# Kernel tuning notes

Measured on AMD Instinct MI355X. Metric: run time of the kernel, lower is better.

Reference implementation:

```python
import jax, jax.numpy as jnp
import numpy as np

N_EXPERTS = 6
TOP_K = 2
AUX_COEFF = 0.01
W_SCALE = 0.02  # keep activations in a sane range with random weights


def setup_inputs() -> dict:
    key = jax.random.key(0)
    k1, k2, k3, k4 = jax.random.split(key, 4)
    B, T, D, H = 4, 2048, 1024, 4096
    x = jax.random.normal(k1, (B, T, D), dtype=jnp.float32)
    w_router = jax.random.normal(k2, (D, N_EXPERTS), dtype=jnp.float32) * W_SCALE
    w1 = jax.random.normal(k3, (N_EXPERTS, D, H), dtype=jnp.float32) * W_SCALE
    w2 = jax.random.normal(k4, (N_EXPERTS, H, D), dtype=jnp.float32) * W_SCALE
    return {"x": x, "w_router": w_router, "w1": w1, "w2": w2}


def reference(x, w_router, w1, w2):
    B, T, D = x.shape
    x_flat = x.reshape(-1, D)                              # (N, D)
    router_logits = x_flat @ w_router                      # (N, E)
    router_probs = jax.nn.softmax(router_logits, axis=-1)
    top_probs, top_idx = jax.lax.top_k(router_probs, TOP_K)  # (N, K)
    top_probs = top_probs / jnp.sum(top_probs, axis=-1, keepdims=True)
    # combine weights per (token, expert): sum over k slots hitting expert e
    onehot = jax.nn.one_hot(top_idx, N_EXPERTS, dtype=x.dtype)  # (N, K, E)
    comb = jnp.einsum('nke,nk->ne', onehot, top_probs)          # (N, E)
    out = jnp.zeros_like(x_flat)
    for e in range(N_EXPERTS):
        h = jax.nn.gelu(x_flat @ w1[e], approximate=False)      # (N, H)
        out = out + comb[:, e:e + 1] * (h @ w2[e])              # (N, D)
    tokens_per_expert = jnp.mean(router_probs, axis=0)          # (E,)
    uniform = jnp.full_like(tokens_per_expert, 1.0 / N_EXPERTS)
    aux_loss = AUX_COEFF * jnp.mean((tokens_per_expert - uniform) ** 2)
    return out.reshape(B, T, D), aux_loss
```

## Files before the change

### kernel.cpp

```cpp
#include <hip/hip_runtime.h>

#define N_TOK 8192
#define DDIM  1024
#define HDIM  4096
#define NEXP  6
#define RBLOCKS (N_TOK / 4)
#define SBLOCKS 32

typedef unsigned short ushort_t;
typedef __bf16 bf16_t;
typedef bf16_t bf16x8 __attribute__((ext_vector_type(8)));
typedef float f32x4 __attribute__((ext_vector_type(4)));

typedef const __attribute__((address_space(1))) void* gptr_t;
typedef __attribute__((address_space(3))) void* lptr_t;

__device__ __forceinline__ void g2l16(const void* g, void* l) {
    __builtin_amdgcn_global_load_lds((gptr_t)g, (lptr_t)l, 16, 0, 0);
}

__device__ __forceinline__ ushort_t f2bf(float f) {
    unsigned int u = __float_as_uint(f);
    unsigned int r = (u + 0x7FFFu + ((u >> 16) & 1u)) >> 16;
    return (ushort_t)r;
}

__global__ void transpose_bf16_kernel(const float* __restrict__ src, ushort_t* __restrict__ dst,
                                      int R, int C) {
    __shared__ float tile[32][33];
    size_t msz = (size_t)R * C;
    src += (size_t)blockIdx.z * msz;
    dst += (size_t)blockIdx.z * msz;
    int c0 = blockIdx.x * 32, r0 = blockIdx.y * 32;
    int tx = threadIdx.x & 31, ty = threadIdx.x >> 5;
#pragma unroll
    for (int i = 0; i < 4; ++i)
        tile[ty + 8 * i][tx] = src[(size_t)(r0 + ty + 8 * i) * C + c0 + tx];
    __syncthreads();
#pragma unroll
    for (int i = 0; i < 4; ++i)
        dst[(size_t)(c0 + ty + 8 * i) * R + r0 + tx] = f2bf(tile[tx][ty + 8 * i]);
}

__global__ void router_kernel(const float* __restrict__ x, const float* __restrict__ wr,
                              ushort_t* __restrict__ xb,
                              int* __restrict__ tok_e, float* __restrict__ tok_w,
                              float* __restrict__ part_p, int* __restrict__ part_c) {
    __shared__ float bsum[NEXP];
    __shared__ int bcnt[NEXP];
    int wid = threadIdx.x >> 6, l = threadIdx.x & 63;
    if (threadIdx.x < NEXP) { bsum[threadIdx.x] = 0.f; bcnt[threadIdx.x] = 0; }
    __syncthreads();
    int t = blockIdx.x * 4 + wid;
    const float* xr = x + (size_t)t * DDIM;
    ushort_t* xbr = xb + (size_t)t * DDIM;
    float acc[NEXP] = {0.f, 0.f, 0.f, 0.f, 0.f, 0.f};
#pragma unroll
    for (int c = 0; c < 4; ++c) {
        int k0 = c * 256 + l * 4;
        float4 xv = *(const float4*)(xr + k0);
        union { ushort_t u[4]; uint2 v; } ob;
        ob.u[0] = f2bf(xv.x); ob.u[1] = f2bf(xv.y); ob.u[2] = f2bf(xv.z); ob.u[3] = f2bf(xv.w);
        *(uint2*)(xbr + k0) = ob.v;
        float wv[24];
#pragma unroll
        for (int q = 0; q < 6; ++q)
            *(float4*)(wv + 4 * q) = *(const float4*)(wr + (size_t)k0 * NEXP + 4 * q);
        float xa[4] = {xv.x, xv.y, xv.z, xv.w};
#pragma unroll
        for (int r = 0; r < 4; ++r)
#pragma unroll
            for (int e = 0; e < NEXP; ++e) acc[e] += xa[r] * wv[r * NEXP + e];
    }
#pragma unroll
    for (int e = 0; e < NEXP; ++e)
#pragma unroll
        for (int d = 32; d >= 1; d >>= 1) acc[e] += __shfl_xor(acc[e], d);
    if (l == 0) {
        float m = acc[0];
#pragma unroll
        for (int e = 1; e < NEXP; ++e) m = fmaxf(m, acc[e]);
        float p[NEXP], s = 0.f;
#pragma unroll
        for (int e = 0; e < NEXP; ++e) { p[e] = expf(acc[e] - m); s += p[e]; }
        float inv = 1.0f / s;
#pragma unroll
        for (int e = 0; e < NEXP; ++e) p[e] *= inv;
        int i1 = 0; float b1 = p[0];
#pragma unroll
        for (int e = 1; e < NEXP; ++e) if (p[e] > b1) { b1 = p[e]; i1 = e; }
        int i2 = -1; float b2 = -1.f;
#pragma unroll
        for (int e = 0; e < NEXP; ++e) if (e != i1 && p[e] > b2) { b2 = p[e]; i2 = e; }
        float swn = 1.0f / (b1 + b2);
        tok_e[2 * t] = i1; tok_e[2 * t + 1] = i2;
        tok_w[2 * t] = b1 * swn; tok_w[2 * t + 1] = b2 * swn;
        atomicAdd(&bcnt[i1], 1);
        atomicAdd(&bcnt[i2], 1);
#pragma unroll
        for (int e = 0; e < NEXP; ++e) atomicAdd(&bsum[e], p[e]);
    }
    __syncthreads();
    if (threadIdx.x < NEXP) {
        part_p[(size_t)blockIdx.x * NEXP + threadIdx.x] = bsum[threadIdx.x];
        part_c[(size_t)blockIdx.x * NEXP + threadIdx.x] = bcnt[threadIdx.x];
    }
}

__global__ void finalize_kernel(const float* __restrict__ part_p, const int* __restrict__ part_c,
                                int* __restrict__ counts, int* __restrict__ offs,
                                float* __restrict__ aux_out) {
    __shared__ float redp[NEXP][4];
    __shared__ int redc[NEXP][4];
    int tid = threadIdx.x, wid = tid >> 6, l = tid & 63;
    float myp[NEXP] = {0.f, 0.f, 0.f, 0.f, 0.f, 0.f};
    int myc[NEXP] = {0, 0, 0, 0, 0, 0};
    for (int b = tid; b < RBLOCKS; b += 256) {
#pragma unroll
        for (int e = 0; e < NEXP; ++e) {
            myp[e] += part_p[(size_t)b * NEXP + e];
            myc[e] += part_c[(size_t)b * NEXP + e];
        }
    }
#pragma unroll
    for (int e = 0; e < NEXP; ++e) {
#pragma unroll
        for (int d = 32; d >= 1; d >>= 1) {
            myp[e] += __shfl_xor(myp[e], d);
            myc[e] += __shfl_xor(myc[e], d);
        }
        if (l == 0) { redp[e][wid] = myp[e]; redc[e][wid] = myc[e]; }
    }
    __syncthreads();
    if (tid == 0) {
        int o = 0;
        float s = 0.f;
        for (int e = 0; e < NEXP; ++e) {
            int c = redc[e][0] + redc[e][1] + redc[e][2] + redc[e][3];
            float ps = redp[e][0] + redp[e][1] + redp[e][2] + redp[e][3];
            counts[e] = c;
            offs[e] = o;
            o += c;
            float d = ps / (float)N_TOK - (1.0f / 6.0f);
            s += d * d;
        }
        offs[NEXP] = o;
        aux_out[0] = 0.01f * (s / 6.0f);
    }
}

__global__ void scatter_kernel(const int* __restrict__ tok_e, const float* __restrict__ tok_w,
                               const int* __restrict__ offs, int* __restrict__ cursors,
                               int* __restrict__ slot_token, float* __restrict__ slot_w) {
    __shared__ int lcnt[NEXP], lbase[NEXP];
    int tid = threadIdx.x;
    if (tid < NEXP) lcnt[tid] = 0;
    __syncthreads();
    int t = blockIdx.x * 256 + tid;
    int e0 = tok_e[2 * t], e1 = tok_e[2 * t + 1];
    int r0 = atomicAdd(&lcnt[e0], 1);
    int r1 = atomicAdd(&lcnt[e1], 1);
    __syncthreads();
    if (tid < NEXP) lbase[tid] = atomicAdd(&cursors[tid], lcnt[tid]);
    __syncthreads();
    int i0 = offs[e0] + lbase[e0] + r0;
    slot_token[i0] = t; slot_w[i0] = tok_w[2 * t];
    int i1 = offs[e1] + lbase[e1] + r1;
    slot_token[i1] = t; slot_w[i1] = tok_w[2 * t + 1];
}


#define STAGE(BI, KTE) do { \
    ushort_t* bA_ = sbase + (BI) * 12288; \
    ushort_t* bB_ = bA_ + 4096; \
    g2l16(A + aoff[0] + (KTE),   bA_ + wid * 512); \
    g2l16(A + aoff[1] + (KTE),   bA_ + 2048 + wid * 512); \
    g2l16(Bte + boff[0] + (KTE), bB_ + wid * 512); \
    g2l16(Bte + boff[1] + (KTE), bB_ + 2048 + wid * 512); \
    g2l16(Bte + boff[2] + (KTE), bB_ + 4096 + wid * 512); \
    g2l16(Bte + boff[3] + (KTE), bB_ + 6144 + wid * 512); \
  } while (0)

template <int LAYER>
__global__ __launch_bounds__(256, 2)
void moe_gemm_kernel(const ushort_t* __restrict__ A, const ushort_t* __restrict__ Bt,
                     ushort_t* __restrict__ Hout, float* __restrict__ Out,
                     const int* __restrict__ slot_token, const float* __restrict__ slot_w,
                     const int* __restrict__ offs, const int* __restrict__ counts) {
    constexpr int Kd = (LAYER == 1) ? DDIM : HDIM;
    constexpr int Nd = (LAYER == 1) ? HDIM : DDIM;
    constexpr int NT = Kd / 32;
    extern __shared__ __align__(16) char smem[];
    ushort_t* sbase = (ushort_t*)smem;

    const int e = blockIdx.z;
    const int cnt = counts[e];
    const int mbase = blockIdx.y * 128;
    if (mbase >= cnt) return;
    const int nbase = blockIdx.x * 256;
    const int off = offs[e];
    const ushort_t* Bte = Bt + (size_t)e * ((size_t)Nd * Kd);

    const int tid = threadIdx.x;
    const int wid = tid >> 6, l = tid & 63;

    size_t aoff[2];
#pragma unroll
    for (int j = 0; j < 2; ++j) {
        int p = j * 256 + tid;
        int row = p >> 2, slot = p & 3;
        int cs = slot ^ ((row >> 1) & 3);
        int gr = mbase + row;
        int grc = gr < cnt - 1 ? gr : cnt - 1;
        size_t arow = (LAYER == 1) ? (size_t)slot_token[off + grc] * DDIM
                                   : (size_t)(off + grc) * HDIM;
        aoff[j] = arow + (size_t)cs * 8;
    }
    size_t boff[4];
#pragma unroll
    for (int j = 0; j < 4; ++j) {
        int p = j * 256 + tid;
        int row = p >> 2, slot = p & 3;
        int cs = slot ^ ((row >> 1) & 3);
        boff[j] = (size_t)(nbase + row) * Kd + (size_t)cs * 8;
    }

    const int lm = l & 15, kg = l >> 4;
    const int wm = (wid & 1) * 64, wn = (wid >> 1) * 128;
    int aOffs[4], bOffs[8];
#pragma unroll
    for (int fr = 0; fr < 4; ++fr) {
        int ar = wm + fr * 16 + lm;
        aOffs[fr] = ar * 64 + ((kg ^ ((ar >> 1) & 3)) << 4);
    }
#pragma unroll
    for (int fr = 0; fr < 8; ++fr) {
        int br = wn + fr * 16 + lm;
        bOffs[fr] = br * 64 + ((kg ^ ((br >> 1) & 3)) << 4);
    }

    f32x4 acc[4][8] = {};

    STAGE(0, 0);
    STAGE(1, 32);
    asm volatile("s_waitcnt vmcnt(6)" ::: "memory");
    __builtin_amdgcn_sched_barrier(0);
    __builtin_amdgcn_s_barrier();

    int rb = 0;
    for (int t = 0; t < NT; ++t) {
        int sb = rb + 2; if (sb >= 3) sb -= 3;
        if (t + 2 < NT) STAGE(sb, (t + 2) * 32);
        const char* bA = (const char*)(sbase + rb * 12288);
        const char* bB = bA + 8192;
        bf16x8 af[4], bfv[8];
#pragma unroll
        for (int fr = 0; fr < 4; ++fr) af[fr] = *(const bf16x8*)(bA + aOffs[fr]);
#pragma unroll
        for (int fr = 0; fr < 8; ++fr) bfv[fr] = *(const bf16x8*)(bB + bOffs[fr]);
#pragma unroll
        for (int i = 0; i < 4; ++i)
#pragma unroll
            for (int n = 0; n < 8; ++n)
                acc[i][n] = __builtin_amdgcn_mfma_f32_16x16x32_bf16(af[i], bfv[n], acc[i][n], 0, 0, 0);
        if (t < NT - 1) {
            if (t + 3 <= NT) { asm volatile("s_waitcnt vmcnt(6)" ::: "memory"); }
            else             { asm volatile("s_waitcnt vmcnt(0)" ::: "memory"); }
            __builtin_amdgcn_sched_barrier(0);
            __builtin_amdgcn_s_barrier();
        }
        rb = rb + 1; if (rb >= 3) rb -= 3;
    }

    if (LAYER == 1) {
#pragma unroll
        for (int i = 0; i < 4; ++i) {
#pragma unroll
            for (int r = 0; r < 4; ++r) {
                int grow = mbase + wm + i * 16 + kg * 4 + r;
                if (grow < cnt) {
                    size_t hbase = (size_t)(off + grow) * HDIM + nbase + wn + lm;
#pragma unroll
                    for (int n = 0; n < 8; ++n) {
                        float v = acc[i][n][r];
                        float u = -1.5957691216f * v * (1.0f + 0.044715f * v * v);
                        float g = v / (1.0f + __expf(u));
                        Hout[hbase + n * 16] = f2bf(g);
                    }
                }
            }
        }
    } else {
#pragma unroll
        for (int i = 0; i < 4; ++i) {
#pragma unroll
            for (int r = 0; r < 4; ++r) {
                int grow = mbase + wm + i * 16 + kg * 4 + r;
                if (grow < cnt) {
                    int si = off + grow;
                    int tok = slot_token[si];
                    float wgt = slot_w[si];
                    float* obase = Out + (size_t)tok * DDIM + nbase + wn + lm;
#pragma unroll
                    for (int n = 0; n < 8; ++n)
                        atomicAdd(obase + n * 16, wgt * acc[i][n][r]);
                }
            }
        }
    }
}
#undef STAGE

extern "C" void kernel_launch(void* const* d_in, const int* in_sizes, int n_in,
                              void* d_out, int out_size, void* d_ws, size_t ws_size,
                              hipStream_t stream) {
    const float* x  = (const float*)d_in[0];
    const float* wr = (const float*)d_in[1];
    const float* w1 = (const float*)d_in[2];
    const float* w2 = (const float*)d_in[3];
    float* out = (float*)d_out;

    char* ws = (char*)d_ws;
    size_t o = 0;
    ushort_t* xb   = (ushort_t*)(ws + o); o += (size_t)N_TOK * DDIM * 2;
    ushort_t* w1t  = (ushort_t*)(ws + o); o += (size_t)NEXP * HDIM * DDIM * 2;
    ushort_t* w2t  = (ushort_t*)(ws + o); o += (size_t)NEXP * DDIM * HDIM * 2;
    ushort_t* hbuf = (ushort_t*)(ws + o); o += (size_t)2 * N_TOK * HDIM * 2;
    int*   tok_e   = (int*)(ws + o);   o += (size_t)N_TOK * 2 * 4;
    float* tok_w   = (float*)(ws + o); o += (size_t)N_TOK * 2 * 4;
    int*   slot_token = (int*)(ws + o);   o += (size_t)2 * N_TOK * 4;
    float* slot_w     = (float*)(ws + o); o += (size_t)2 * N_TOK * 4;
    float* part_p  = (float*)(ws + o); o += (size_t)RBLOCKS * NEXP * 4;
    int*   part_c  = (int*)(ws + o);   o += (size_t)RBLOCKS * NEXP * 4;
    int*   counts  = (int*)(ws + o);   o += 32;
    int*   cursors = (int*)(ws + o);   o += 32;
    int*   offs    = (int*)(ws + o);   o += 32;

    hipMemsetAsync(d_out, 0, (size_t)out_size * sizeof(float), stream);
    hipMemsetAsync(cursors, 0, 32, stream);

    hipFuncSetAttribute((const void*)moe_gemm_kernel<1>, hipFuncAttributeMaxDynamicSharedMemorySize, 73728);
    hipFuncSetAttribute((const void*)moe_gemm_kernel<2>, hipFuncAttributeMaxDynamicSharedMemorySize, 73728);

    router_kernel<<<dim3(RBLOCKS), 256, 0, stream>>>(x, wr, xb, tok_e, tok_w, part_p, part_c);
    transpose_bf16_kernel<<<dim3(HDIM / 32, DDIM / 32, NEXP), 256, 0, stream>>>(w1, w1t, DDIM, HDIM);
    transpose_bf16_kernel<<<dim3(DDIM / 32, HDIM / 32, NEXP), 256, 0, stream>>>(w2, w2t, HDIM, DDIM);
    finalize_kernel<<<dim3(1), 256, 0, stream>>>(part_p, part_c, counts, offs, out + (size_t)N_TOK * DDIM);
    scatter_kernel<<<dim3(SBLOCKS), 256, 0, stream>>>(tok_e, tok_w, offs, cursors, slot_token, slot_w);
    moe_gemm_kernel<1><<<dim3(HDIM / 256, N_TOK / 128, NEXP), 256, 73728, stream>>>(
        xb, w1t, hbuf, nullptr, slot_token, slot_w, offs, counts);
    moe_gemm_kernel<2><<<dim3(DDIM / 256, N_TOK / 128, NEXP), 256, 73728, stream>>>(
        hbuf, w2t, nullptr, out, slot_token, slot_w, offs, counts);
}
```

Measured before the change: 486.5 us.

## Enlarge MoE GEMM tile to 256x256 with four-stage LDS pipeline

Doubles the M tile of both expert GEMMs from 128 to 256 rows, so each warp computes a 128x128 sub-tile with 64 accumulators. The LDS ring grows from three to four stages (128 KB), with deeper vmcnt waits, and MFMA issue is wrapped in s_setprio. The aim is more reuse per loaded tile and better latency hiding. The cost is occupancy dropping to one block per CU, much higher register pressure, and more padding waste on partially filled expert tiles.

```diff
diff --git a/kernel.cpp b/kernel.cpp
--- a/kernel.cpp
+++ b/kernel.cpp
@@ -171,18 +171,19 @@
 
 
 #define STAGE(BI, KTE) do { \
-    ushort_t* bA_ = sbase + (BI) * 12288; \
-    ushort_t* bB_ = bA_ + 4096; \
-    g2l16(A + aoff[0] + (KTE),   bA_ + wid * 512); \
-    g2l16(A + aoff[1] + (KTE),   bA_ + 2048 + wid * 512); \
-    g2l16(Bte + boff[0] + (KTE), bB_ + wid * 512); \
-    g2l16(Bte + boff[1] + (KTE), bB_ + 2048 + wid * 512); \
-    g2l16(Bte + boff[2] + (KTE), bB_ + 4096 + wid * 512); \
-    g2l16(Bte + boff[3] + (KTE), bB_ + 6144 + wid * 512); \
+    ushort_t* b_ = sbase + (BI) * 16384; \
+    g2l16(A + aoff[0] + (KTE),   b_ + wid * 512); \
+    g2l16(A + aoff[1] + (KTE),   b_ + 2048 + wid * 512); \
+    g2l16(A + aoff[2] + (KTE),   b_ + 4096 + wid * 512); \
+    g2l16(A + aoff[3] + (KTE),   b_ + 6144 + wid * 512); \
+    g2l16(Bte + boff[0] + (KTE), b_ + 8192 + wid * 512); \
+    g2l16(Bte + boff[1] + (KTE), b_ + 10240 + wid * 512); \
+    g2l16(Bte + boff[2] + (KTE), b_ + 12288 + wid * 512); \
+    g2l16(Bte + boff[3] + (KTE), b_ + 14336 + wid * 512); \
   } while (0)
 
 template <int LAYER>
-__global__ __launch_bounds__(256, 2)
+__global__ __launch_bounds__(256, 1)
 void moe_gemm_kernel(const ushort_t* __restrict__ A, const ushort_t* __restrict__ Bt,
                      ushort_t* __restrict__ Hout, float* __restrict__ Out,
                      const int* __restrict__ slot_token, const float* __restrict__ slot_w,
@@ -195,7 +196,7 @@
 
     const int e = blockIdx.z;
     const int cnt = counts[e];
-    const int mbase = blockIdx.y * 128;
+    const int mbase = blockIdx.y * 256;
     if (mbase >= cnt) return;
     const int nbase = blockIdx.x * 256;
     const int off = offs[e];
@@ -204,9 +205,9 @@
     const int tid = threadIdx.x;
     const int wid = tid >> 6, l = tid & 63;
 
-    size_t aoff[2];
-#pragma unroll
-    for (int j = 0; j < 2; ++j) {
+    size_t aoff[4];
+#pragma unroll
+    for (int j = 0; j < 4; ++j) {
         int p = j * 256 + tid;
         int row = p >> 2, slot = p & 3;
         int cs = slot ^ ((row >> 1) & 3);
@@ -226,55 +227,56 @@
     }
 
     const int lm = l & 15, kg = l >> 4;
-    const int wm = (wid & 1) * 64, wn = (wid >> 1) * 128;
-    int aOffs[4], bOffs[8];
-#pragma unroll
-    for (int fr = 0; fr < 4; ++fr) {
+    const int wm = (wid & 1) * 128, wn = (wid >> 1) * 128;
+    int aOffs[8], bOffs[8];
+#pragma unroll
+    for (int fr = 0; fr < 8; ++fr) {
         int ar = wm + fr * 16 + lm;
         aOffs[fr] = ar * 64 + ((kg ^ ((ar >> 1) & 3)) << 4);
-    }
-#pragma unroll
-    for (int fr = 0; fr < 8; ++fr) {
         int br = wn + fr * 16 + lm;
-        bOffs[fr] = br * 64 + ((kg ^ ((br >> 1) & 3)) << 4);
-    }
-
-    f32x4 acc[4][8] = {};
+        bOffs[fr] = 16384 + br * 64 + ((kg ^ ((br >> 1) & 3)) << 4);
+    }
+
+    f32x4 acc[8][8] = {};
 
     STAGE(0, 0);
     STAGE(1, 32);
-    asm volatile("s_waitcnt vmcnt(6)" ::: "memory");
+    STAGE(2, 64);
+    asm volatile("s_waitcnt vmcnt(16)" ::: "memory");
     __builtin_amdgcn_sched_barrier(0);
     __builtin_amdgcn_s_barrier();
 
     int rb = 0;
     for (int t = 0; t < NT; ++t) {
-        int sb = rb + 2; if (sb >= 3) sb -= 3;
-        if (t + 2 < NT) STAGE(sb, (t + 2) * 32);
-        const char* bA = (const char*)(sbase + rb * 12288);
-        const char* bB = bA + 8192;
-        bf16x8 af[4], bfv[8];
-#pragma unroll
-        for (int fr = 0; fr < 4; ++fr) af[fr] = *(const bf16x8*)(bA + aOffs[fr]);
-#pragma unroll
-        for (int fr = 0; fr < 8; ++fr) bfv[fr] = *(const bf16x8*)(bB + bOffs[fr]);
-#pragma unroll
-        for (int i = 0; i < 4; ++i)
+        int sb = rb + 3; if (sb >= 4) sb -= 4;
+        if (t + 3 < NT) STAGE(sb, (t + 3) * 32);
+        const char* bA = (const char*)sbase + rb * 32768;
+        bf16x8 af[8], bfv[8];
+#pragma unroll
+        for (int fr = 0; fr < 8; ++fr) {
+            af[fr]  = *(const bf16x8*)(bA + aOffs[fr]);
+            bfv[fr] = *(const bf16x8*)(bA + bOffs[fr]);
+        }
+        __builtin_amdgcn_s_setprio(1);
+#pragma unroll
+        for (int i = 0; i < 8; ++i)
 #pragma unroll
             for (int n = 0; n < 8; ++n)
                 acc[i][n] = __builtin_amdgcn_mfma_f32_16x16x32_bf16(af[i], bfv[n], acc[i][n], 0, 0, 0);
+        __builtin_amdgcn_s_setprio(0);
         if (t < NT - 1) {
-            if (t + 3 <= NT) { asm volatile("s_waitcnt vmcnt(6)" ::: "memory"); }
-            else             { asm volatile("s_waitcnt vmcnt(0)" ::: "memory"); }
+            if (t < NT - 3)       { asm volatile("s_waitcnt vmcnt(16)" ::: "memory"); }
+            else if (t == NT - 3) { asm volatile("s_waitcnt vmcnt(8)"  ::: "memory"); }
+            else                  { asm volatile("s_waitcnt vmcnt(0)"  ::: "memory"); }
             __builtin_amdgcn_sched_barrier(0);
             __builtin_amdgcn_s_barrier();
         }
-        rb = rb + 1; if (rb >= 3) rb -= 3;
+        rb = rb + 1; if (rb >= 4) rb -= 4;
     }
 
     if (LAYER == 1) {
 #pragma unroll
-        for (int i = 0; i < 4; ++i) {
+        for (int i = 0; i < 8; ++i) {
 #pragma unroll
             for (int r = 0; r < 4; ++r) {
                 int grow = mbase + wm + i * 16 + kg * 4 + r;
@@ -292,7 +294,7 @@
         }
     } else {
 #pragma unroll
-        for (int i = 0; i < 4; ++i) {
+        for (int i = 0; i < 8; ++i) {
 #pragma unroll
             for (int r = 0; r < 4; ++r) {
                 int grow = mbase + wm + i * 16 + kg * 4 + r;
@@ -339,16 +341,16 @@
     hipMemsetAsync(d_out, 0, (size_t)out_size * sizeof(float), stream);
     hipMemsetAsync(cursors, 0, 32, stream);
 
-    hipFuncSetAttribute((const void*)moe_gemm_kernel<1>, hipFuncAttributeMaxDynamicSharedMemorySize, 73728);
-    hipFuncSetAttribute((const void*)moe_gemm_kernel<2>, hipFuncAttributeMaxDynamicSharedMemorySize, 73728);
+    hipFuncSetAttribute((const void*)moe_gemm_kernel<1>, hipFuncAttributeMaxDynamicSharedMemorySize, 131072);
+    hipFuncSetAttribute((const void*)moe_gemm_kernel<2>, hipFuncAttributeMaxDynamicSharedMemorySize, 131072);
 
     router_kernel<<<dim3(RBLOCKS), 256, 0, stream>>>(x, wr, xb, tok_e, tok_w, part_p, part_c);
     transpose_bf16_kernel<<<dim3(HDIM / 32, DDIM / 32, NEXP), 256, 0, stream>>>(w1, w1t, DDIM, HDIM);
     transpose_bf16_kernel<<<dim3(DDIM / 32, HDIM / 32, NEXP), 256, 0, stream>>>(w2, w2t, HDIM, DDIM);
     finalize_kernel<<<dim3(1), 256, 0, stream>>>(part_p, part_c, counts, offs, out + (size_t)N_TOK * DDIM);
     scatter_kernel<<<dim3(SBLOCKS), 256, 0, stream>>>(tok_e, tok_w, offs, cursors, slot_token, slot_w);
-    moe_gemm_kernel<1><<<dim3(HDIM / 256, N_TOK / 128, NEXP), 256, 73728, stream>>>(
+    moe_gemm_kernel<1><<<dim3(HDIM / 256, N_TOK / 256, NEXP), 256, 131072, stream>>>(
         xb, w1t, hbuf, nullptr, slot_token, slot_w, offs, counts);
-    moe_gemm_kernel<2><<<dim3(DDIM / 256, N_TOK / 128, NEXP), 256, 73728, stream>>>(
+    moe_gemm_kernel<2><<<dim3(DDIM / 256, N_TOK / 256, NEXP), 256, 131072, stream>>>(
         hbuf, w2t, nullptr, out, slot_token, slot_w, offs, counts);
 }
```

Result: slower. 602.1 us (+23.7%).

## Compact MoE GEMM grid via per-expert m-block table and XCD-aware remap

Applied to the files above, without the earlier changes.

Finalize now builds a compact table of (expert, m-block) pairs, and both grouped GEMMs launch a fixed grid of 134 m-blocks instead of 6×64 mostly-empty blocks. Block IDs are remapped so consecutive tiles sharing an expert and m-block land on the same XCD (stride-8 interleave), aiming for better L2 reuse of weights and activations. The change also raises wave priority around the MFMA loop with s_setprio. The remap adds a table lookup per block and assumes the total number of m-blocks never exceeds 134.

```diff
diff --git a/kernel.cpp b/kernel.cpp
--- a/kernel.cpp
+++ b/kernel.cpp
@@ -6,6 +6,7 @@
 #define NEXP  6
 #define RBLOCKS (N_TOK / 4)
 #define SBLOCKS 32
+#define MAXMB 134
 
 typedef unsigned short ushort_t;
 typedef __bf16 bf16_t;
@@ -109,6 +110,7 @@
 
 __global__ void finalize_kernel(const float* __restrict__ part_p, const int* __restrict__ part_c,
                                 int* __restrict__ counts, int* __restrict__ offs,
+                                int* __restrict__ mbt,
                                 float* __restrict__ aux_out) {
     __shared__ float redp[NEXP][4];
     __shared__ int redc[NEXP][4];
@@ -135,16 +137,20 @@
     if (tid == 0) {
         int o = 0;
         float s = 0.f;
+        int idx = 0;
         for (int e = 0; e < NEXP; ++e) {
             int c = redc[e][0] + redc[e][1] + redc[e][2] + redc[e][3];
             float ps = redp[e][0] + redp[e][1] + redp[e][2] + redp[e][3];
             counts[e] = c;
             offs[e] = o;
             o += c;
+            int nmb = (c + 127) >> 7;
+            for (int m = 0; m < nmb; ++m) mbt[idx++] = (e << 16) | m;
             float d = ps / (float)N_TOK - (1.0f / 6.0f);
             s += d * d;
         }
         offs[NEXP] = o;
+        for (; idx < MAXMB; ++idx) mbt[idx] = -1;
         aux_out[0] = 0.01f * (s / 6.0f);
     }
 }
@@ -186,18 +192,25 @@
 void moe_gemm_kernel(const ushort_t* __restrict__ A, const ushort_t* __restrict__ Bt,
                      ushort_t* __restrict__ Hout, float* __restrict__ Out,
                      const int* __restrict__ slot_token, const float* __restrict__ slot_w,
-                     const int* __restrict__ offs, const int* __restrict__ counts) {
+                     const int* __restrict__ offs, const int* __restrict__ counts,
+                     const int* __restrict__ mbt) {
     constexpr int Kd = (LAYER == 1) ? DDIM : HDIM;
     constexpr int Nd = (LAYER == 1) ? HDIM : DDIM;
+    constexpr int NX = Nd / 256;
+    constexpr int NXSH = (LAYER == 1) ? 4 : 2;
     constexpr int NT = Kd / 32;
     extern __shared__ __align__(16) char smem[];
     ushort_t* sbase = (ushort_t*)smem;
 
-    const int e = blockIdx.z;
+    const int F = blockIdx.y * NX + blockIdx.x;
+    const int q8 = (NX * MAXMB) >> 3;
+    const int L = (F & 7) * q8 + (F >> 3);
+    const int mv = mbt[L >> NXSH];
+    if (mv < 0) return;
+    const int e = mv >> 16;
+    const int mbase = (mv & 0xffff) << 7;
+    const int nbase = (L & (NX - 1)) << 8;
     const int cnt = counts[e];
-    const int mbase = blockIdx.y * 128;
-    if (mbase >= cnt) return;
-    const int nbase = blockIdx.x * 256;
     const int off = offs[e];
     const ushort_t* Bte = Bt + (size_t)e * ((size_t)Nd * Kd);
 
@@ -258,11 +271,13 @@
         for (int fr = 0; fr < 4; ++fr) af[fr] = *(const bf16x8*)(bA + aOffs[fr]);
 #pragma unroll
         for (int fr = 0; fr < 8; ++fr) bfv[fr] = *(const bf16x8*)(bB + bOffs[fr]);
+        __builtin_amdgcn_s_setprio(1);
 #pragma unroll
         for (int i = 0; i < 4; ++i)
 #pragma unroll
             for (int n = 0; n < 8; ++n)
                 acc[i][n] = __builtin_amdgcn_mfma_f32_16x16x32_bf16(af[i], bfv[n], acc[i][n], 0, 0, 0);
+        __builtin_amdgcn_s_setprio(0);
         if (t < NT - 1) {
             if (t + 3 <= NT) { asm volatile("s_waitcnt vmcnt(6)" ::: "memory"); }
             else             { asm volatile("s_waitcnt vmcnt(0)" ::: "memory"); }
@@ -335,6 +350,7 @@
     int*   counts  = (int*)(ws + o);   o += 32;
     int*   cursors = (int*)(ws + o);   o += 32;
     int*   offs    = (int*)(ws + o);   o += 32;
+    int*   mbt     = (int*)(ws + o);   o += 4 * 160;
 
     hipMemsetAsync(d_out, 0, (size_t)out_size * sizeof(float), stream);
     hipMemsetAsync(cursors, 0, 32, stream);
@@ -345,10 +361,11 @@
     router_kernel<<<dim3(RBLOCKS), 256, 0, stream>>>(x, wr, xb, tok_e, tok_w, part_p, part_c);
     transpose_bf16_kernel<<<dim3(HDIM / 32, DDIM / 32, NEXP), 256, 0, stream>>>(w1, w1t, DDIM, HDIM);
     transpose_bf16_kernel<<<dim3(DDIM / 32, HDIM / 32, NEXP), 256, 0, stream>>>(w2, w2t, HDIM, DDIM);
-    finalize_kernel<<<dim3(1), 256, 0, stream>>>(part_p, part_c, counts, offs, out + (size_t)N_TOK * DDIM);
+    finalize_kernel<<<dim3(1), 256, 0, stream>>>(part_p, part_c, counts, offs, mbt,
+                                                 out + (size_t)N_TOK * DDIM);
     scatter_kernel<<<dim3(SBLOCKS), 256, 0, stream>>>(tok_e, tok_w, offs, cursors, slot_token, slot_w);
-    moe_gemm_kernel<1><<<dim3(HDIM / 256, N_TOK / 128, NEXP), 256, 73728, stream>>>(
-        xb, w1t, hbuf, nullptr, slot_token, slot_w, offs, counts);
-    moe_gemm_kernel<2><<<dim3(DDIM / 256, N_TOK / 128, NEXP), 256, 73728, stream>>>(
-        hbuf, w2t, nullptr, out, slot_token, slot_w, offs, counts);
-}
+    moe_gemm_kernel<1><<<dim3(HDIM / 256, MAXMB), 256, 73728, stream>>>(
+        xb, w1t, hbuf, nullptr, slot_token, slot_w, offs, counts, mbt);
+    moe_gemm_kernel<2><<<dim3(DDIM / 256, MAXMB), 256, 73728, stream>>>(
+        hbuf, w2t, nullptr, out, slot_token, slot_w, offs, counts, mbt);
+}
```

Measured after the change: 504.1 us. 3.6% more time.
